# Kernel optimization log

Hardware: AMD Instinct MI355X
Metric: run time of the kernel (lower is better)

The kernel has to match this reference:

```python
import jax, jax.numpy as jnp
import numpy as np

N, C, F = 131072, 1000, 512

def setup_inputs() -> dict:
    key = jax.random.key(0)
    k1, k2 = jax.random.split(key)
    x = jax.random.normal(k1, (N, F), dtype=jnp.float32)
    W = jax.random.normal(k2, (C, F), dtype=jnp.float32) * (1.0 / np.sqrt(F))
    b = jnp.zeros((C,), dtype=jnp.float32)
    similarity_init = jnp.zeros((C, F), dtype=jnp.float32)
    class_counts_init = jnp.zeros((C,), dtype=jnp.float32)
    return {"x": x, "W": W, "b": b,
            "similarity_init": similarity_init,
            "class_counts_init": class_counts_init}

def reference(x, W, b, similarity_init, class_counts_init):
    # fc1: [N,F] @ [F,C] + b -> [N,C]
    logits = jnp.einsum('nf,cf->nc', x, W) + b
    max_values = jnp.argmax(logits, axis=1)  # [N] int, class routing
    # scatter-add counts: class_counts[idx] += 1 per row
    class_counts = class_counts_init + jax.ops.segment_sum(
        jnp.ones((x.shape[0],), dtype=x.dtype), max_values, num_segments=class_counts_init.shape[0])
    # scatter-add features: similarity[idx] += x[row]
    similarity = similarity_init + jax.ops.segment_sum(
        x, max_values, num_segments=similarity_init.shape[0])
    # per-class mean (classes with zero count give inf/nan, same as torch 0/0)
    similarity_weight = similarity / class_counts[:, None]
    att_out_repair = x * 0.9
    return att_out_repair, class_counts, similarity, similarity_weight
```

## Files before the change

kernel.cpp:

```cpp
#include <hip/hip_runtime.h>

#define N_F 512
#define N_C 1000
#define BM 128
#define BN 256
#define BK 64
#define MARGIN 0.0625f
#define NCAND 16

using short8  = __attribute__((ext_vector_type(8))) short;
using floatx4 = __attribute__((ext_vector_type(4))) float;

__device__ __forceinline__ unsigned short f2bf(float f) {
    unsigned u = __float_as_uint(f);
    unsigned r = u + 0x7FFFu + ((u >> 16) & 1u);
    return (unsigned short)(r >> 16);
}
__device__ __forceinline__ unsigned fkey(float f) {
    unsigned u = __float_as_uint(f);
    return (u & 0x80000000u) ? ~u : (u | 0x80000000u);
}
__device__ __forceinline__ float kinv(unsigned k) {
    unsigned u = (k & 0x80000000u) ? (k & 0x7FFFFFFFu) : ~k;
    return __uint_as_float(u);
}
__device__ __forceinline__ void gload_lds16(const void* g, void* l) {
    __builtin_amdgcn_global_load_lds((const __attribute__((address_space(1))) void*)g,
                                     (__attribute__((address_space(3))) void*)l, 16, 0, 0);
}

__global__ __launch_bounds__(256) void conv_x_kernel(
    const float* __restrict__ x, unsigned short* __restrict__ xbf,
    float* __restrict__ att, long n8)
{
    const long stride = (long)gridDim.x * 256;
    for (long i = (long)blockIdx.x * 256 + threadIdx.x; i < n8; i += stride) {
        const float4 a = ((const float4*)x)[2 * i];
        const float4 c = ((const float4*)x)[2 * i + 1];
        if (att) {
            float4 o0, o1;
            o0.x = 0.9f * a.x; o0.y = 0.9f * a.y; o0.z = 0.9f * a.z; o0.w = 0.9f * a.w;
            o1.x = 0.9f * c.x; o1.y = 0.9f * c.y; o1.z = 0.9f * c.z; o1.w = 0.9f * c.w;
            ((float4*)att)[2 * i]     = o0;
            ((float4*)att)[2 * i + 1] = o1;
        }
        short8 s;
        s[0] = (short)f2bf(a.x); s[1] = (short)f2bf(a.y);
        s[2] = (short)f2bf(a.z); s[3] = (short)f2bf(a.w);
        s[4] = (short)f2bf(c.x); s[5] = (short)f2bf(c.y);
        s[6] = (short)f2bf(c.z); s[7] = (short)f2bf(c.w);
        ((short8*)xbf)[i] = s;
    }
}

__global__ __launch_bounds__(256) void conv_w_kernel(
    const float* __restrict__ W, unsigned short* __restrict__ wbf,
    int* __restrict__ wlCount)
{
    if (blockIdx.x == 0 && threadIdx.x == 0) wlCount[0] = 0;
    const int r = blockIdx.x;
    const int t = threadIdx.x;
    unsigned short v0 = 0, v1 = 0;
    if (r < N_C) {
        const float2 w2 = ((const float2*)(W + (size_t)r * N_F))[t];
        v0 = f2bf(w2.x); v1 = f2bf(w2.y);
    }
    wbf[(size_t)r * N_F + 2 * t]     = v0;
    wbf[(size_t)r * N_F + 2 * t + 1] = v1;
}

__global__ __launch_bounds__(256) void att_fix_kernel(
    const float* __restrict__ x, float* __restrict__ att, long n4)
{
    const long stride = (long)gridDim.x * 256;
    for (long i = (long)blockIdx.x * 256 + threadIdx.x; i < n4; i += stride) {
        const float4 a = ((const float4*)x)[i];
        float4 o;
        o.x = 0.9f * a.x; o.y = 0.9f * a.y; o.z = 0.9f * a.z; o.w = 0.9f * a.w;
        ((float4*)att)[i] = o;
    }
}

__global__ __launch_bounds__(256, 2) void gemm_argmax_kernel(
    const unsigned short* __restrict__ xbf, const unsigned short* __restrict__ wbf,
    const float* __restrict__ b, int* __restrict__ candG,
    int* __restrict__ labels, int* __restrict__ wlCount, int* __restrict__ worklist)
{
    __shared__ unsigned short As[BM][BK];
    __shared__ unsigned short Bs[BN][BK];
    __shared__ unsigned runmaxkey[BM];
    __shared__ int candCnt[BM];
    __shared__ float candVal[BM][NCAND];
    __shared__ int   candCls[BM][NCAND];

    const int tid  = threadIdx.x;
    const int rowBase = blockIdx.x * BM;
    const int lane = tid & 63;
    const int w    = tid >> 6;
    const int wm   = (w >> 1) * 64;
    const int wn   = (w & 1) * 128;
    const int quad = lane >> 4;
    const int l16  = lane & 15;

    if (tid < BM) { runmaxkey[tid] = 0u; candCnt[tid] = 0; }

    const int srow   = w * 8 + (lane >> 3);
    const int schunk = (lane & 7) ^ (lane >> 3);
    const unsigned short* aG = xbf + (size_t)(rowBase + srow) * N_F + schunk * 8;
    const unsigned short* bG = wbf + (size_t)srow * N_F + schunk * 8;

    for (int ctg = 0; ctg < 4; ++ctg) {
        floatx4 acc[4][8];
        #pragma unroll
        for (int mt = 0; mt < 4; ++mt)
            #pragma unroll
            for (int nt = 0; nt < 8; ++nt)
                acc[mt][nt] = (floatx4){0.f, 0.f, 0.f, 0.f};

        const int ctBase = ctg * BN;
        const unsigned short* bGc = bG + (size_t)ctBase * N_F;

        for (int k0 = 0; k0 < N_F; k0 += BK) {
            __syncthreads();
            #pragma unroll
            for (int p = 0; p < 4; ++p)
                gload_lds16(aG  + (size_t)p * 32 * N_F + k0, &As[p * 32 + w * 8][0]);
            #pragma unroll
            for (int p = 0; p < 8; ++p)
                gload_lds16(bGc + (size_t)p * 32 * N_F + k0, &Bs[p * 32 + w * 8][0]);
            __syncthreads();
            #pragma unroll
            for (int chunk = 0; chunk < 2; ++chunk) {
                const int pcol = ((chunk * 4 + quad) ^ (l16 & 7)) * 8;
                short8 af[4], bfr[8];
                #pragma unroll
                for (int mt = 0; mt < 4; ++mt)
                    af[mt] = *(const short8*)&As[wm + mt * 16 + l16][pcol];
                #pragma unroll
                for (int nt = 0; nt < 8; ++nt)
                    bfr[nt] = *(const short8*)&Bs[wn + nt * 16 + l16][pcol];
                #pragma unroll
                for (int mt = 0; mt < 4; ++mt)
                    #pragma unroll
                    for (int nt = 0; nt < 8; ++nt)
                        acc[mt][nt] = __builtin_amdgcn_mfma_f32_16x16x32_bf16(
                            af[mt], bfr[nt], acc[mt][nt], 0, 0, 0);
            }
        }

        float bv[8]; bool valid[8]; int cls[8];
        #pragma unroll
        for (int nt = 0; nt < 8; ++nt) {
            const int c = ctBase + wn + nt * 16 + l16;
            cls[nt] = c; valid[nt] = (c < N_C);
            bv[nt]  = valid[nt] ? b[c] : 0.f;
        }
        #pragma unroll
        for (int mt = 0; mt < 4; ++mt) {
            #pragma unroll
            for (int i = 0; i < 4; ++i) {
                float m = -3e38f;
                #pragma unroll
                for (int nt = 0; nt < 8; ++nt) {
                    const float v = valid[nt] ? (acc[mt][nt][i] + bv[nt]) : -3e38f;
                    m = fmaxf(m, v);
                }
                m = fmaxf(m, __shfl_xor(m, 1, 64));
                m = fmaxf(m, __shfl_xor(m, 2, 64));
                m = fmaxf(m, __shfl_xor(m, 4, 64));
                m = fmaxf(m, __shfl_xor(m, 8, 64));
                if (l16 == 0) {
                    const int r = wm + mt * 16 + quad * 4 + i;
                    atomicMax(&runmaxkey[r], fkey(m));
                }
            }
        }
        __syncthreads();
        #pragma unroll
        for (int mt = 0; mt < 4; ++mt) {
            #pragma unroll
            for (int i = 0; i < 4; ++i) {
                const int r = wm + mt * 16 + quad * 4 + i;
                const float thresh = kinv(runmaxkey[r]) - MARGIN;
                #pragma unroll
                for (int nt = 0; nt < 8; ++nt) {
                    if (valid[nt]) {
                        const float v = acc[mt][nt][i] + bv[nt];
                        if (v > thresh) {
                            const int s = atomicAdd(&candCnt[r], 1);
                            if (s < NCAND) { candVal[r][s] = v; candCls[r][s] = cls[nt]; }
                        }
                    }
                }
            }
        }
    }

    __syncthreads();
    if (tid < BM) {
        const int R = rowBase + tid;
        const int raw = candCnt[tid];
        if (raw > NCAND) {
            const int pos = atomicAdd(wlCount, 1);
            worklist[pos] = R;
            candG[(size_t)R * 8] = -1;
        } else {
            const float thresh = kinv(runmaxkey[tid]) - MARGIN;
            int cnt = 0; int keep[7];
            for (int s = 0; s < raw; ++s) {
                if (candVal[tid][s] > thresh) {
                    if (cnt < 7) keep[cnt] = candCls[tid][s];
                    ++cnt;
                }
            }
            if (cnt == 1) {
                labels[R] = keep[0];
            } else {
                const int pos = atomicAdd(wlCount, 1);
                worklist[pos] = R;
                candG[(size_t)R * 8] = (cnt > 7) ? -1 : cnt;
                const int m = cnt < 7 ? cnt : 7;
                for (int s = 0; s < m; ++s) candG[(size_t)R * 8 + 1 + s] = keep[s];
            }
        }
    }
}

__global__ __launch_bounds__(256) void label_kernel(
    const float* __restrict__ x, const float* __restrict__ W,
    const float* __restrict__ b, const int* __restrict__ candG,
    const int* __restrict__ wlCount, const int* __restrict__ worklist,
    int* __restrict__ labels)
{
    const int nAmb   = wlCount[0];
    const int waveId = blockIdx.x * 4 + (threadIdx.x >> 6);
    const int nWaves = gridDim.x * 4;
    const int lane   = threadIdx.x & 63;

    for (int idx = waveId; idx < nAmb; idx += nWaves) {
        const int row = worklist[idx];
        const int cnt = candG[(size_t)row * 8];
        const float* xr = x + (size_t)row * N_F;
        const float4 x0 = *(const float4*)&xr[lane * 8];
        const float4 x1 = *(const float4*)&xr[lane * 8 + 4];
        double best = -1e300; int bestc = 0x7fffffff;
        const bool all = (cnt < 0);
        const int ncand = all ? N_C : cnt;
        for (int s = 0; s < ncand; ++s) {
            const int c = all ? s : candG[(size_t)row * 8 + 1 + s];
            const float* wc = W + (size_t)c * N_F + lane * 8;
            const float4 w0 = *(const float4*)&wc[0];
            const float4 w1 = *(const float4*)&wc[4];
            double p = (double)x0.x * w0.x + (double)x0.y * w0.y
                     + (double)x0.z * w0.z + (double)x0.w * w0.w
                     + (double)x1.x * w1.x + (double)x1.y * w1.y
                     + (double)x1.z * w1.z + (double)x1.w * w1.w;
            #pragma unroll
            for (int off = 1; off < 64; off <<= 1) p += __shfl_xor(p, off, 64);
            p += (double)b[c];
            if (p > best || (p == best && c < bestc)) { best = p; bestc = c; }
        }
        if (lane == 0) labels[row] = bestc;
    }
}

__global__ __launch_bounds__(256) void scatter_kernel(
    const float* __restrict__ x, const int* __restrict__ labels,
    const float* __restrict__ sim_init, const float* __restrict__ cnt_init,
    float* __restrict__ out_counts, float* __restrict__ out_sim,
    float* __restrict__ out_w, int N)
{
    __shared__ float psum[4][N_F];
    __shared__ int ptot[4];
    const int c    = blockIdx.x;
    const int t    = threadIdx.x;
    const int w    = t >> 6;
    const int lane = t & 63;

    float a0=0.f,a1=0.f,a2=0.f,a3=0.f,a4=0.f,a5=0.f,a6=0.f,a7=0.f;
    int total = 0;
    const int quarter = N >> 2;
    const int qbeg = w * quarter;
    for (int base = 0; base < quarter; base += 256) {
        const int4 l4 = *(const int4*)&labels[qbeg + base + lane * 4];
        unsigned long long m0 = __ballot(l4.x == c);
        unsigned long long m1 = __ballot(l4.y == c);
        unsigned long long m2 = __ballot(l4.z == c);
        unsigned long long m3 = __ballot(l4.w == c);
        #define POP(mm, sub) \
        while (mm) { int bit = __ffsll(mm) - 1; mm &= mm - 1; \
            const float* xr = &x[(size_t)(qbeg + base + bit * 4 + sub) * N_F + lane * 8]; \
            const float4 v0 = *(const float4*)&xr[0]; \
            const float4 v1 = *(const float4*)&xr[4]; \
            a0 += v0.x; a1 += v0.y; a2 += v0.z; a3 += v0.w; \
            a4 += v1.x; a5 += v1.y; a6 += v1.z; a7 += v1.w; ++total; }
        POP(m0, 0) POP(m1, 1) POP(m2, 2) POP(m3, 3)
        #undef POP
    }
    float* ps = &psum[w][lane * 8];
    ps[0]=a0; ps[1]=a1; ps[2]=a2; ps[3]=a3; ps[4]=a4; ps[5]=a5; ps[6]=a6; ps[7]=a7;
    if (lane == 0) ptot[w] = total;
    __syncthreads();

    const int f = t * 2;
    const float s0p = psum[0][f]   + psum[1][f]   + psum[2][f]   + psum[3][f];
    const float s1p = psum[0][f+1] + psum[1][f+1] + psum[2][f+1] + psum[3][f+1];
    const float countf = cnt_init[c] + (float)(ptot[0] + ptot[1] + ptot[2] + ptot[3]);
    if (t == 0) out_counts[c] = countf;
    const float2 si = *(const float2*)&sim_init[(size_t)c * N_F + f];
    const float s0 = s0p + si.x, s1 = s1p + si.y;
    float2 so; so.x = s0; so.y = s1;
    *(float2*)&out_sim[(size_t)c * N_F + f] = so;
    float2 wo; wo.x = s0 / countf; wo.y = s1 / countf;
    *(float2*)&out_w[(size_t)c * N_F + f] = wo;
}

extern "C" void kernel_launch(void* const* d_in, const int* in_sizes, int n_in,
                              void* d_out, int out_size, void* d_ws, size_t ws_size,
                              hipStream_t stream) {
    const float* x        = (const float*)d_in[0];
    const float* W        = (const float*)d_in[1];
    const float* b        = (const float*)d_in[2];
    const float* sim_init = (const float*)d_in[3];
    const float* cnt_init = (const float*)d_in[4];
    const int N = in_sizes[0] / N_F;

    float* out_att    = (float*)d_out;
    float* out_counts = out_att + (size_t)N * N_F;
    float* out_sim    = out_counts + N_C;
    float* out_w      = out_sim + (size_t)N_C * N_F;

    int* labels   = (int*)d_ws;
    int* candG    = labels + N;
    int* wlCount  = candG + (size_t)N * 8;
    int* worklist = wlCount + 4;

    const size_t baseWs    = (size_t)N * 4 + (size_t)N * 32 + 16 + (size_t)N * 4;
    const size_t xbfBytes  = (size_t)N * N_F * 2;
    const size_t wbfBytes  = (size_t)1024 * N_F * 2;
    const bool bigws = ws_size >= baseWs + xbfBytes + wbfBytes;

    unsigned short *xbf, *wbf;
    if (bigws) {
        xbf = (unsigned short*)((char*)d_ws + baseWs);
        wbf = xbf + (size_t)N * N_F;
    } else {
        xbf = (unsigned short*)d_out;
        wbf = xbf + (size_t)N * N_F;
    }

    conv_x_kernel<<<2048, 256, 0, stream>>>(x, xbf, bigws ? out_att : nullptr,
                                            (long)N * N_F / 8);
    conv_w_kernel<<<1024, 256, 0, stream>>>(W, wbf, wlCount);
    gemm_argmax_kernel<<<N / BM, 256, 0, stream>>>(xbf, wbf, b, candG,
                                                   labels, wlCount, worklist);
    label_kernel<<<4096, 256, 0, stream>>>(x, W, b, candG, wlCount, worklist, labels);
    scatter_kernel<<<N_C, 256, 0, stream>>>(x, labels, sim_init, cnt_init,
                                            out_counts, out_sim, out_w, N);
    if (!bigws)
        att_fix_kernel<<<2048, 256, 0, stream>>>(x, out_att, (long)N * N_F / 4);
}
```

Before: 812.1 us.

## Double-buffer GEMM LDS tiles with BK=32 and widen candidate lists

Restructures the GEMM main loop into a double-buffered LDS pipeline with BK halved to 32. The next K slice, or the next class tile's first slice, is prefetched while MFMAs run on the current buffer, so only one barrier is needed per step instead of two. It also raises the per-row candidate capacity to 24 and stores every kept candidate with a stride of 32. This is meant to reduce full 1000-class fallbacks in the label kernel. The cost is that the XOR swizzle is dropped, which risks LDS bank conflicts, and the workspace grows so the bigws path for xbf may no longer fit.

Result: slower. 880.8 us (+8.5%).

```diff
diff --git a/kernel.cpp b/kernel.cpp
--- a/kernel.cpp
+++ b/kernel.cpp
@@ -4,9 +4,10 @@
 #define N_C 1000
 #define BM 128
 #define BN 256
-#define BK 64
+#define BK 32
 #define MARGIN 0.0625f
-#define NCAND 16
+#define NCAND 24
+#define CSTRIDE 32
 
 using short8  = __attribute__((ext_vector_type(8))) short;
 using floatx4 = __attribute__((ext_vector_type(4))) float;
@@ -86,8 +87,8 @@
     const float* __restrict__ b, int* __restrict__ candG,
     int* __restrict__ labels, int* __restrict__ wlCount, int* __restrict__ worklist)
 {
-    __shared__ unsigned short As[BM][BK];
-    __shared__ unsigned short Bs[BN][BK];
+    __shared__ unsigned short As[2][BM][BK];
+    __shared__ unsigned short Bs[2][BN][BK];
     __shared__ unsigned runmaxkey[BM];
     __shared__ int candCnt[BM];
     __shared__ float candVal[BM][NCAND];
@@ -104,10 +105,18 @@
 
     if (tid < BM) { runmaxkey[tid] = 0u; candCnt[tid] = 0; }
 
-    const int srow   = w * 8 + (lane >> 3);
-    const int schunk = (lane & 7) ^ (lane >> 3);
-    const unsigned short* aG = xbf + (size_t)(rowBase + srow) * N_F + schunk * 8;
-    const unsigned short* bG = wbf + (size_t)srow * N_F + schunk * 8;
+    const int lrow = lane >> 2;
+    const int lcol = (lane & 3) * 8;
+    const unsigned short* aG = xbf + (size_t)(rowBase + lrow) * N_F + lcol;
+    const unsigned short* bG = wbf + (size_t)lrow * N_F + lcol;
+
+    #pragma unroll
+    for (int p = 0; p < 2; ++p)
+        gload_lds16(aG + (size_t)(w * 32 + p * 16) * N_F, &As[0][w * 32 + p * 16][0]);
+    #pragma unroll
+    for (int p = 0; p < 4; ++p)
+        gload_lds16(bG + (size_t)(w * 64 + p * 16) * N_F, &Bs[0][w * 64 + p * 16][0]);
+    __syncthreads();
 
     for (int ctg = 0; ctg < 4; ++ctg) {
         floatx4 acc[4][8];
@@ -118,34 +127,35 @@
                 acc[mt][nt] = (floatx4){0.f, 0.f, 0.f, 0.f};
 
         const int ctBase = ctg * BN;
-        const unsigned short* bGc = bG + (size_t)ctBase * N_F;
-
-        for (int k0 = 0; k0 < N_F; k0 += BK) {
+
+        for (int ks = 0; ks < 16; ++ks) {
+            const int cur = ks & 1;
+            if (!(ctg == 3 && ks == 15)) {
+                const int nk  = (ks == 15) ? 0 : (ks + 1) * BK;
+                const int nct = (ks == 15) ? ctBase + BN : ctBase;
+                #pragma unroll
+                for (int p = 0; p < 2; ++p)
+                    gload_lds16(aG + (size_t)(w * 32 + p * 16) * N_F + nk,
+                                &As[cur ^ 1][w * 32 + p * 16][0]);
+                #pragma unroll
+                for (int p = 0; p < 4; ++p)
+                    gload_lds16(bG + (size_t)(nct + w * 64 + p * 16) * N_F + nk,
+                                &Bs[cur ^ 1][w * 64 + p * 16][0]);
+            }
+            short8 af[4], bfr[8];
+            #pragma unroll
+            for (int mt = 0; mt < 4; ++mt)
+                af[mt] = *(const short8*)&As[cur][wm + mt * 16 + l16][quad * 8];
+            #pragma unroll
+            for (int nt = 0; nt < 8; ++nt)
+                bfr[nt] = *(const short8*)&Bs[cur][wn + nt * 16 + l16][quad * 8];
+            #pragma unroll
+            for (int mt = 0; mt < 4; ++mt)
+                #pragma unroll
+                for (int nt = 0; nt < 8; ++nt)
+                    acc[mt][nt] = __builtin_amdgcn_mfma_f32_16x16x32_bf16(
+                        af[mt], bfr[nt], acc[mt][nt], 0, 0, 0);
             __syncthreads();
-            #pragma unroll
-            for (int p = 0; p < 4; ++p)
-                gload_lds16(aG  + (size_t)p * 32 * N_F + k0, &As[p * 32 + w * 8][0]);
-            #pragma unroll
-            for (int p = 0; p < 8; ++p)
-                gload_lds16(bGc + (size_t)p * 32 * N_F + k0, &Bs[p * 32 + w * 8][0]);
-            __syncthreads();
-            #pragma unroll
-            for (int chunk = 0; chunk < 2; ++chunk) {
-                const int pcol = ((chunk * 4 + quad) ^ (l16 & 7)) * 8;
-                short8 af[4], bfr[8];
-                #pragma unroll
-                for (int mt = 0; mt < 4; ++mt)
-                    af[mt] = *(const short8*)&As[wm + mt * 16 + l16][pcol];
-                #pragma unroll
-                for (int nt = 0; nt < 8; ++nt)
-                    bfr[nt] = *(const short8*)&Bs[wn + nt * 16 + l16][pcol];
-                #pragma unroll
-                for (int mt = 0; mt < 4; ++mt)
-                    #pragma unroll
-                    for (int nt = 0; nt < 8; ++nt)
-                        acc[mt][nt] = __builtin_amdgcn_mfma_f32_16x16x32_bf16(
-                            af[mt], bfr[nt], acc[mt][nt], 0, 0, 0);
-            }
         }
 
         float bv[8]; bool valid[8]; int cls[8];
@@ -194,33 +204,32 @@
                 }
             }
         }
-    }
-
-    __syncthreads();
+        __syncthreads();
+    }
+
     if (tid < BM) {
         const int R = rowBase + tid;
         const int raw = candCnt[tid];
         if (raw > NCAND) {
             const int pos = atomicAdd(wlCount, 1);
             worklist[pos] = R;
-            candG[(size_t)R * 8] = -1;
+            candG[(size_t)R * CSTRIDE] = -1;
         } else {
             const float thresh = kinv(runmaxkey[tid]) - MARGIN;
-            int cnt = 0; int keep[7];
+            int cnt = 0, firstKept = 0;
             for (int s = 0; s < raw; ++s) {
                 if (candVal[tid][s] > thresh) {
-                    if (cnt < 7) keep[cnt] = candCls[tid][s];
+                    if (cnt == 0) firstKept = candCls[tid][s];
+                    candG[(size_t)R * CSTRIDE + 1 + cnt] = candCls[tid][s];
                     ++cnt;
                 }
             }
             if (cnt == 1) {
-                labels[R] = keep[0];
+                labels[R] = firstKept;
             } else {
                 const int pos = atomicAdd(wlCount, 1);
                 worklist[pos] = R;
-                candG[(size_t)R * 8] = (cnt > 7) ? -1 : cnt;
-                const int m = cnt < 7 ? cnt : 7;
-                for (int s = 0; s < m; ++s) candG[(size_t)R * 8 + 1 + s] = keep[s];
+                candG[(size_t)R * CSTRIDE] = cnt;
             }
         }
     }
@@ -239,7 +248,7 @@
 
     for (int idx = waveId; idx < nAmb; idx += nWaves) {
         const int row = worklist[idx];
-        const int cnt = candG[(size_t)row * 8];
+        const int cnt = candG[(size_t)row * CSTRIDE];
         const float* xr = x + (size_t)row * N_F;
         const float4 x0 = *(const float4*)&xr[lane * 8];
         const float4 x1 = *(const float4*)&xr[lane * 8 + 4];
@@ -247,7 +256,7 @@
         const bool all = (cnt < 0);
         const int ncand = all ? N_C : cnt;
         for (int s = 0; s < ncand; ++s) {
-            const int c = all ? s : candG[(size_t)row * 8 + 1 + s];
+            const int c = all ? s : candG[(size_t)row * CSTRIDE + 1 + s];
             const float* wc = W + (size_t)c * N_F + lane * 8;
             const float4 w0 = *(const float4*)&wc[0];
             const float4 w1 = *(const float4*)&wc[4];
@@ -332,10 +341,10 @@
 
     int* labels   = (int*)d_ws;
     int* candG    = labels + N;
-    int* wlCount  = candG + (size_t)N * 8;
+    int* wlCount  = candG + (size_t)N * CSTRIDE;
     int* worklist = wlCount + 4;
 
-    const size_t baseWs    = (size_t)N * 4 + (size_t)N * 32 + 16 + (size_t)N * 4;
+    const size_t baseWs    = (size_t)N * 4 + (size_t)N * CSTRIDE * 4 + 16 + (size_t)N * 4;
     const size_t xbfBytes  = (size_t)N * N_F * 2;
     const size_t wbfBytes  = (size_t)1024 * N_F * 2;
     const bool bigws = ws_size >= baseWs + xbfBytes + wbfBytes;
```
